# Optimization experiments

Hardware: AMD Instinct MI355X
Metric: run time of the kernel (lower is better)

The kernel has to match this reference:

```python
import jax, jax.numpy as jnp
import numpy as np


def setup_inputs() -> dict:
    key = jax.random.key(0)
    k1, k2, k3, k4 = jax.random.split(key, 4)
    TOKENS, IN_F, OUT_F = 4096, 4096, 11008
    x = jax.random.normal(k1, (TOKENS, IN_F), dtype=jnp.float32)
    # int8-valued weights stored in fp32 buffer, as in the torch module
    quantized_weight = jax.random.randint(k2, (OUT_F, IN_F), -128, 128).astype(jnp.float32)
    # per-output-channel scales, positive, small (like max|w|/127)
    weight_scales = (jax.random.uniform(k3, (OUT_F, 1), dtype=jnp.float32) * 0.03 + 0.001)
    bias = jax.random.normal(k4, (OUT_F,), dtype=jnp.float32)
    return {"x": x, "quantized_weight": quantized_weight,
            "weight_scales": weight_scales, "bias": bias}


def reference(x, quantized_weight, weight_scales, bias):
    # dequantize: per-channel scale broadcast over in_features
    weight = quantized_weight * weight_scales  # [out, in]
    # F.linear: x @ weight.T + bias
    return jnp.dot(x, weight.T) + bias
```

## Files before the change

kernel.cpp:

```cpp
#include <hip/hip_runtime.h>
#include <hip/hip_bf16.h>


typedef __attribute__((ext_vector_type(4))) int   i32x4;
typedef __attribute__((ext_vector_type(4))) float f32x4;
typedef __attribute__((ext_vector_type(4))) unsigned int u32x4;

__device__ static inline unsigned int pack4(int q0, int q1, int q2, int q3) {
    return (unsigned)(q0 & 255) | ((unsigned)(q1 & 255) << 8) |
           ((unsigned)(q2 & 255) << 16) | ((unsigned)(q3 & 255) << 24);
}

__global__ void w_to_i8(const float* __restrict__ in,
                        u32x4* __restrict__ out, long n16) {
    const long stride = (long)gridDim.x * blockDim.x;
    for (long i = (long)blockIdx.x * blockDim.x + threadIdx.x; i < n16; i += stride) {
        const f32x4* p = reinterpret_cast<const f32x4*>(in) + i * 4;
        u32x4 o;
#pragma unroll
        for (int v = 0; v < 4; ++v) {
            f32x4 f = p[v];
            o[v] = pack4(__float2int_rn(f[0]), __float2int_rn(f[1]),
                         __float2int_rn(f[2]), __float2int_rn(f[3]));
        }
        out[i] = o;
    }
}

__global__ void x_quant_i8(const float* __restrict__ x,
                           unsigned int* __restrict__ xq,
                           float* __restrict__ sx, int K) {
    const int row = blockIdx.x;
    const int tid = threadIdx.x;
    const float* xr = x + (size_t)row * K;
    float m = 0.f;
    for (int b = tid * 16; b < K; b += blockDim.x * 16) {
        const f32x4* p = (const f32x4*)(xr + b);
#pragma unroll
        for (int v = 0; v < 4; ++v) {
            f32x4 f = p[v];
            m = fmaxf(m, fmaxf(fmaxf(fabsf(f[0]), fabsf(f[1])),
                               fmaxf(fabsf(f[2]), fabsf(f[3]))));
        }
    }
#pragma unroll
    for (int off = 32; off; off >>= 1) m = fmaxf(m, __shfl_xor(m, off));
    __shared__ float red[8];
    if ((tid & 63) == 0) red[tid >> 6] = m;
    __syncthreads();
    const int nw = blockDim.x >> 6;
    m = red[0];
    for (int i = 1; i < nw; ++i) m = fmaxf(m, red[i]);
    const float inv = (m > 0.f) ? 127.0f / m : 0.f;
    if (tid == 0) sx[row] = m * (1.0f / 127.0f);
    for (int b = tid * 16; b < K; b += blockDim.x * 16) {
        const f32x4* p = (const f32x4*)(xr + b);
        u32x4 o;
#pragma unroll
        for (int v = 0; v < 4; ++v) {
            f32x4 f = p[v];
            int q0 = min(127, max(-127, __float2int_rn(f[0] * inv)));
            int q1 = min(127, max(-127, __float2int_rn(f[1] * inv)));
            int q2 = min(127, max(-127, __float2int_rn(f[2] * inv)));
            int q3 = min(127, max(-127, __float2int_rn(f[3] * inv)));
            o[v] = pack4(q0, q1, q2, q3);
        }
        *reinterpret_cast<u32x4*>((char*)xq + (size_t)row * K + b) = o;
    }
}


#define GLOAD16(src, dst) __builtin_amdgcn_global_load_lds( \
    (const __attribute__((address_space(1))) void*)(src),   \
    (__attribute__((address_space(3))) void*)(dst), 16, 0, 0)

#define FENCE() asm volatile("" ::: "memory")
#define BAR()  do { FENCE(); __builtin_amdgcn_s_barrier(); FENCE(); } while (0)
#define WAIT_VM(n) asm volatile("s_waitcnt vmcnt(" #n ")" ::: "memory")
#define WAIT_LGKM0() asm volatile("s_waitcnt lgkmcnt(0)" ::: "memory")
#define SCHED0() __builtin_amdgcn_sched_barrier(0)

__global__ __launch_bounds__(512, 2)
void qlinear_gemm_i8v2(const char* __restrict__ A,
                       const char* __restrict__ B,
                       const float* __restrict__ sx,
                       const float* __restrict__ scales,
                       const float* __restrict__ bias,
                       float* __restrict__ C,
                       int M, int N, int K, int nbx) {
    __shared__ __align__(128) char smem[131072];

    const int tid  = threadIdx.x;
    const int lane = tid & 63;
    const int wid  = tid >> 6;
    const int wr   = wid >> 2;
    const int wc   = wid & 3;

    const int nwg = gridDim.x;
    const int q = nwg >> 3, r = nwg & 7;
    const int xcd = blockIdx.x & 7, boff_ = blockIdx.x >> 3;
    const int swz = (xcd < r ? xcd * (q + 1) : r * (q + 1) + (xcd - r) * q) + boff_;
    const int bcol = swz % nbx;
    const int brow = swz / nbx;

    const char* Ag = A + (size_t)brow * 256 * K;
    const char* Bg = B + (size_t)bcol * 256 * K;

    size_t sA[2], sB[2];
#pragma unroll
    for (int g = 0; g < 2; ++g) {
        const int c = tid + g * 512, rl = c >> 3, j = c & 7;
        const int rowA = ((rl >> 6) << 7) + (rl & 63);
        const int rowB = ((rl >> 5) << 6) + (rl & 31);
        sA[g] = (size_t)rowA * K + ((j ^ (rl & 7)) << 4);
        sB[g] = (size_t)rowB * K + ((j ^ (rl & 7)) << 4);
    }
    const int ld0 = tid * 16;

    auto stageA = [&](int rg, int h, int t) {
        const char* G = Ag + (size_t)h * 64 * K + (size_t)t * 128;
        char* base = smem + rg * 32768 + h * 16384;
        GLOAD16(G + sA[0], base + ld0);
        GLOAD16(G + sA[1], base + ld0 + 8192);
    };
    auto stageB = [&](int rg, int h, int t) {
        const char* G = Bg + (size_t)h * 32 * K + (size_t)t * 128;
        char* base = smem + 65536 + rg * 32768 + h * 16384;
        GLOAD16(G + sB[0], base + ld0);
        GLOAD16(G + sB[1], base + ld0 + 8192);
    };

    const int px0 = (((lane >> 4) ^ (lane & 7)) << 4);
    const int px1 = (((4 + (lane >> 4)) ^ (lane & 7)) << 4);
    const int arow = (wr * 64 + (lane & 15)) * 128;
    const int brw  = (wc * 32 + (lane & 15)) * 128;

    i32x4 acc[8][4] = {};
    i32x4 a0[8], a1[8], b0[4], b1[4];

    auto rdA = [&](int rg, int mh, i32x4 (&d)[8]) {
        const char* p = smem + rg * 32768 + mh * 16384 + arow;
#pragma unroll
        for (int i = 0; i < 4; ++i) {
            d[i * 2]     = *(const i32x4*)(p + i * 2048 + px0);
            d[i * 2 + 1] = *(const i32x4*)(p + i * 2048 + px1);
        }
    };
    auto rdB = [&](int rg, int nh, i32x4 (&d)[4]) {
        const char* p = smem + 65536 + rg * 32768 + nh * 16384 + brw;
#pragma unroll
        for (int n = 0; n < 2; ++n) {
            d[n * 2]     = *(const i32x4*)(p + n * 2048 + px0);
            d[n * 2 + 1] = *(const i32x4*)(p + n * 2048 + px1);
        }
    };
    auto mfma16 = [&](const i32x4 (&a)[8], const i32x4 (&b)[4], int mh, int nh) {
#pragma unroll
        for (int i = 0; i < 4; ++i)
#pragma unroll
            for (int n = 0; n < 2; ++n) {
                i32x4& ac = acc[mh * 4 + i][nh * 2 + n];
                ac = __builtin_amdgcn_mfma_i32_16x16x64_i8(a[i * 2], b[n * 2], ac, 0, 0, 0);
                ac = __builtin_amdgcn_mfma_i32_16x16x64_i8(a[i * 2 + 1], b[n * 2 + 1], ac, 0, 0, 0);
            }
    };

    const int NT = K / 128;

    stageA(0, 0, 0); stageB(0, 0, 0); stageA(0, 1, 0); stageB(0, 1, 0);
    stageA(1, 0, 1); stageB(1, 0, 1);
    WAIT_VM(4); BAR();

    for (int t = 0; t < NT - 2; ++t) {
        const int c = t & 1, o = c ^ 1;
        stageA(o, 1, t + 1); stageB(o, 1, t + 1);
        rdA(c, 0, a0); rdB(c, 0, b0); rdB(c, 1, b1);
        WAIT_LGKM0(); SCHED0();
        __builtin_amdgcn_s_setprio(1);
        mfma16(a0, b0, 0, 0);
        mfma16(a0, b1, 0, 1);
        __builtin_amdgcn_s_setprio(0);
        BAR();
        stageA(c, 0, t + 2); stageB(c, 0, t + 2);
        rdA(c, 1, a1);
        WAIT_LGKM0(); SCHED0();
        __builtin_amdgcn_s_setprio(1);
        mfma16(a1, b0, 1, 0);
        mfma16(a1, b1, 1, 1);
        __builtin_amdgcn_s_setprio(0);
        WAIT_VM(4);
        BAR();
    }
    {
        const int c = (NT - 2) & 1, o = c ^ 1;
        stageA(o, 1, NT - 1); stageB(o, 1, NT - 1);
        rdA(c, 0, a0); rdB(c, 0, b0); rdB(c, 1, b1);
        WAIT_LGKM0(); SCHED0();
        __builtin_amdgcn_s_setprio(1);
        mfma16(a0, b0, 0, 0);
        mfma16(a0, b1, 0, 1);
        __builtin_amdgcn_s_setprio(0);
        BAR();
        rdA(c, 1, a1);
        WAIT_LGKM0(); SCHED0();
        __builtin_amdgcn_s_setprio(1);
        mfma16(a1, b0, 1, 0);
        mfma16(a1, b1, 1, 1);
        __builtin_amdgcn_s_setprio(0);
        WAIT_VM(0);
        BAR();
    }
    {
        const int c = (NT - 1) & 1;
        rdA(c, 0, a0); rdB(c, 0, b0); rdB(c, 1, b1);
        WAIT_LGKM0(); SCHED0();
        mfma16(a0, b0, 0, 0);
        mfma16(a0, b1, 0, 1);
        rdA(c, 1, a1);
        WAIT_LGKM0(); SCHED0();
        mfma16(a1, b0, 1, 0);
        mfma16(a1, b1, 1, 1);
    }

    const int lc  = lane & 15;
    const int lr4 = (lane >> 4) * 4;
    float sarr[4], barr[4];
#pragma unroll
    for (int ni = 0; ni < 4; ++ni) {
        const int n = bcol * 256 + wc * 64 + (ni >> 1) * 32 + (ni & 1) * 16 + lc;
        sarr[ni] = scales[n];
        barr[ni] = bias[n];
    }
#pragma unroll
    for (int mi = 0; mi < 8; ++mi) {
        const int mb = brow * 256 + wr * 128 + (mi >> 2) * 64 + (mi & 3) * 16 + lr4;
#pragma unroll
        for (int j = 0; j < 4; ++j) {
            const size_t rowoff = (size_t)(mb + j) * N;
            const float sm = sx[mb + j];
#pragma unroll
            for (int ni = 0; ni < 4; ++ni) {
                const int n = bcol * 256 + wc * 64 + (ni >> 1) * 32 + (ni & 1) * 16 + lc;
                C[rowoff + n] = fmaf((float)acc[mi][ni][j], sm * sarr[ni], barr[ni]);
            }
        }
    }
}

__global__ void qlinear_fallback(const float* __restrict__ A,
                                 const float* __restrict__ B,
                                 const float* __restrict__ scales,
                                 const float* __restrict__ bias,
                                 float* __restrict__ C, int M, int N, int K) {
    __shared__ float As[16][17], Bs[16][17];
    const int tx = threadIdx.x, ty = threadIdx.y;
    const int row = blockIdx.y * 16 + ty;
    const int col = blockIdx.x * 16 + tx;
    float acc = 0.f;
    for (int k0 = 0; k0 < K; k0 += 16) {
        As[ty][tx] = A[(long)row * K + k0 + tx];
        Bs[ty][tx] = B[(long)(blockIdx.x * 16 + ty) * K + k0 + tx];
        __syncthreads();
#pragma unroll
        for (int kk = 0; kk < 16; ++kk) acc += As[ty][kk] * Bs[tx][kk];
        __syncthreads();
    }
    C[(long)row * N + col] = fmaf(acc, scales[col], bias[col]);
}

extern "C" void kernel_launch(void* const* d_in, const int* in_sizes, int n_in,
                              void* d_out, int out_size, void* d_ws, size_t ws_size,
                              hipStream_t stream) {
    const float* x      = (const float*)d_in[0];
    const float* w      = (const float*)d_in[1];
    const float* scales = (const float*)d_in[2];
    const float* bias   = (const float*)d_in[3];
    float* out = (float*)d_out;

    const int N = in_sizes[2];
    const int K = (int)((long)in_sizes[1] / N);
    const int M = (int)((long)in_sizes[0] / K);

    const size_t need = (size_t)M * K + (size_t)N * K + (size_t)M * 4;
    const bool ok = (ws_size >= need) && (M % 256) == 0 && (N % 256) == 0 &&
                    (K % 128) == 0 && (K / 128) >= 3 && (K % 16) == 0;

    if (ok) {
        char* xq = (char*)d_ws;
        char* wq = xq + (size_t)M * K;
        float* sxbuf = (float*)(wq + (size_t)N * K);

        x_quant_i8<<<M, 256, 0, stream>>>(x, (unsigned int*)xq, sxbuf, K);
        w_to_i8<<<2048, 256, 0, stream>>>(w, (u32x4*)wq, (long)N * K / 16);

        const int nbx = N / 256;
        const int nwg = (M / 256) * nbx;
        qlinear_gemm_i8v2<<<nwg, 512, 0, stream>>>(xq, wq, sxbuf, scales, bias,
                                                   out, M, N, K, nbx);
    } else {
        dim3 grid(N / 16, M / 16), blk(16, 16);
        qlinear_fallback<<<grid, blk, 0, stream>>>(x, w, scales, bias, out, M, N, K);
    }
}
```

Baseline: 254.8 us.

## Switch int8 GEMM inner loop to 32x32x32 MFMA tiles

Replaces the 16x16x64 int8 MFMA instructions with 32x32x32 int8 MFMAs, restructuring the LDS read pattern, register fragments and accumulator layout (i32x16) to match. The epilogue is rewritten for the 32x32 output lane mapping and loads the row scales as a vector. The aim is fewer MFMA issues and LDS reads per unit of work and better operand reuse. It changes register pressure and the LDS access pattern, which could affect bank conflicts and occupancy at the 512x2 launch bounds.

Measured after the change: 284.0 us. +11.5%, slower.

```diff
diff --git a/kernel.cpp b/kernel.cpp
--- a/kernel.cpp
+++ b/kernel.cpp
@@ -2,9 +2,10 @@
 #include <hip/hip_bf16.h>
 
 
-typedef __attribute__((ext_vector_type(4))) int   i32x4;
-typedef __attribute__((ext_vector_type(4))) float f32x4;
-typedef __attribute__((ext_vector_type(4))) unsigned int u32x4;
+typedef __attribute__((ext_vector_type(4)))  int   i32x4;
+typedef __attribute__((ext_vector_type(16))) int   i32x16;
+typedef __attribute__((ext_vector_type(4)))  float f32x4;
+typedef __attribute__((ext_vector_type(4)))  unsigned int u32x4;
 
 __device__ static inline unsigned int pack4(int q0, int q1, int q2, int q3) {
     return (unsigned)(q0 & 255) | ((unsigned)(q1 & 255) << 8) |
@@ -81,13 +82,13 @@
 #define SCHED0() __builtin_amdgcn_sched_barrier(0)
 
 __global__ __launch_bounds__(512, 2)
-void qlinear_gemm_i8v2(const char* __restrict__ A,
-                       const char* __restrict__ B,
-                       const float* __restrict__ sx,
-                       const float* __restrict__ scales,
-                       const float* __restrict__ bias,
-                       float* __restrict__ C,
-                       int M, int N, int K, int nbx) {
+void qlinear_gemm_i8x32(const char* __restrict__ A,
+                        const char* __restrict__ B,
+                        const float* __restrict__ sx,
+                        const float* __restrict__ scales,
+                        const float* __restrict__ bias,
+                        float* __restrict__ C,
+                        int M, int N, int K, int nbx) {
     __shared__ __align__(128) char smem[131072];
 
     const int tid  = threadIdx.x;
@@ -130,39 +131,39 @@
         GLOAD16(G + sB[1], base + ld0 + 8192);
     };
 
-    const int px0 = (((lane >> 4) ^ (lane & 7)) << 4);
-    const int px1 = (((4 + (lane >> 4)) ^ (lane & 7)) << 4);
-    const int arow = (wr * 64 + (lane & 15)) * 128;
-    const int brw  = (wc * 32 + (lane & 15)) * 128;
-
-    i32x4 acc[8][4] = {};
-    i32x4 a0[8], a1[8], b0[4], b1[4];
-
-    auto rdA = [&](int rg, int mh, i32x4 (&d)[8]) {
-        const char* p = smem + rg * 32768 + mh * 16384 + arow;
-#pragma unroll
-        for (int i = 0; i < 4; ++i) {
-            d[i * 2]     = *(const i32x4*)(p + i * 2048 + px0);
-            d[i * 2 + 1] = *(const i32x4*)(p + i * 2048 + px1);
-        }
-    };
-    auto rdB = [&](int rg, int nh, i32x4 (&d)[4]) {
-        const char* p = smem + 65536 + rg * 32768 + nh * 16384 + brw;
-#pragma unroll
-        for (int n = 0; n < 2; ++n) {
-            d[n * 2]     = *(const i32x4*)(p + n * 2048 + px0);
-            d[n * 2 + 1] = *(const i32x4*)(p + n * 2048 + px1);
-        }
-    };
-    auto mfma16 = [&](const i32x4 (&a)[8], const i32x4 (&b)[4], int mh, int nh) {
-#pragma unroll
-        for (int i = 0; i < 4; ++i)
-#pragma unroll
-            for (int n = 0; n < 2; ++n) {
-                i32x4& ac = acc[mh * 4 + i][nh * 2 + n];
-                ac = __builtin_amdgcn_mfma_i32_16x16x64_i8(a[i * 2], b[n * 2], ac, 0, 0, 0);
-                ac = __builtin_amdgcn_mfma_i32_16x16x64_i8(a[i * 2 + 1], b[n * 2 + 1], ac, 0, 0, 0);
-            }
+    const int l31 = lane & 31;
+    const int lhi = lane >> 5;
+    const int l7  = lane & 7;
+    int pk[4];
+#pragma unroll
+    for (int ks = 0; ks < 4; ++ks) pk[ks] = ((ks * 2 + lhi) ^ l7) << 4;
+
+    i32x16 acc[4][2] = {};
+    i32x4 am0[4], am1[4], am2[4], am3[4];
+    i32x4 bn0[4], bn1[4];
+
+    auto rdA32 = [&](int rg, int mh, int j, i32x4 (&d)[4]) {
+        const char* p = smem + rg * 32768 + mh * 16384 +
+                        (wr * 64 + j * 32 + l31) * 128;
+#pragma unroll
+        for (int ks = 0; ks < 4; ++ks) d[ks] = *(const i32x4*)(p + pk[ks]);
+    };
+    auto rdB32 = [&](int rg, int n, i32x4 (&d)[4]) {
+        const char* p = smem + 65536 + rg * 32768 + n * 16384 +
+                        (wc * 32 + l31) * 128;
+#pragma unroll
+        for (int ks = 0; ks < 4; ++ks) d[ks] = *(const i32x4*)(p + pk[ks]);
+    };
+    auto mfmaPh = [&](const i32x4 (&x0)[4], const i32x4 (&x1)[4], int mbase) {
+        __builtin_amdgcn_s_setprio(1);
+#pragma unroll
+        for (int ks = 0; ks < 4; ++ks) {
+            acc[mbase][0]     = __builtin_amdgcn_mfma_i32_32x32x32_i8(x0[ks], bn0[ks], acc[mbase][0], 0, 0, 0);
+            acc[mbase][1]     = __builtin_amdgcn_mfma_i32_32x32x32_i8(x0[ks], bn1[ks], acc[mbase][1], 0, 0, 0);
+            acc[mbase + 1][0] = __builtin_amdgcn_mfma_i32_32x32x32_i8(x1[ks], bn0[ks], acc[mbase + 1][0], 0, 0, 0);
+            acc[mbase + 1][1] = __builtin_amdgcn_mfma_i32_32x32x32_i8(x1[ks], bn1[ks], acc[mbase + 1][1], 0, 0, 0);
+        }
+        __builtin_amdgcn_s_setprio(0);
     };
 
     const int NT = K / 128;
@@ -174,74 +175,61 @@
     for (int t = 0; t < NT - 2; ++t) {
         const int c = t & 1, o = c ^ 1;
         stageA(o, 1, t + 1); stageB(o, 1, t + 1);
-        rdA(c, 0, a0); rdB(c, 0, b0); rdB(c, 1, b1);
-        WAIT_LGKM0(); SCHED0();
-        __builtin_amdgcn_s_setprio(1);
-        mfma16(a0, b0, 0, 0);
-        mfma16(a0, b1, 0, 1);
-        __builtin_amdgcn_s_setprio(0);
+        rdA32(c, 0, 0, am0); rdA32(c, 0, 1, am1);
+        rdB32(c, 0, bn0);    rdB32(c, 1, bn1);
+        WAIT_LGKM0(); SCHED0();
+        mfmaPh(am0, am1, 0);
         BAR();
         stageA(c, 0, t + 2); stageB(c, 0, t + 2);
-        rdA(c, 1, a1);
-        WAIT_LGKM0(); SCHED0();
-        __builtin_amdgcn_s_setprio(1);
-        mfma16(a1, b0, 1, 0);
-        mfma16(a1, b1, 1, 1);
-        __builtin_amdgcn_s_setprio(0);
+        rdA32(c, 1, 0, am2); rdA32(c, 1, 1, am3);
+        WAIT_LGKM0(); SCHED0();
+        mfmaPh(am2, am3, 2);
         WAIT_VM(4);
         BAR();
     }
     {
         const int c = (NT - 2) & 1, o = c ^ 1;
         stageA(o, 1, NT - 1); stageB(o, 1, NT - 1);
-        rdA(c, 0, a0); rdB(c, 0, b0); rdB(c, 1, b1);
-        WAIT_LGKM0(); SCHED0();
-        __builtin_amdgcn_s_setprio(1);
-        mfma16(a0, b0, 0, 0);
-        mfma16(a0, b1, 0, 1);
-        __builtin_amdgcn_s_setprio(0);
-        BAR();
-        rdA(c, 1, a1);
-        WAIT_LGKM0(); SCHED0();
-        __builtin_amdgcn_s_setprio(1);
-        mfma16(a1, b0, 1, 0);
-        mfma16(a1, b1, 1, 1);
-        __builtin_amdgcn_s_setprio(0);
+        rdA32(c, 0, 0, am0); rdA32(c, 0, 1, am1);
+        rdB32(c, 0, bn0);    rdB32(c, 1, bn1);
+        WAIT_LGKM0(); SCHED0();
+        mfmaPh(am0, am1, 0);
+        BAR();
+        rdA32(c, 1, 0, am2); rdA32(c, 1, 1, am3);
+        WAIT_LGKM0(); SCHED0();
+        mfmaPh(am2, am3, 2);
         WAIT_VM(0);
         BAR();
     }
     {
         const int c = (NT - 1) & 1;
-        rdA(c, 0, a0); rdB(c, 0, b0); rdB(c, 1, b1);
-        WAIT_LGKM0(); SCHED0();
-        mfma16(a0, b0, 0, 0);
-        mfma16(a0, b1, 0, 1);
-        rdA(c, 1, a1);
-        WAIT_LGKM0(); SCHED0();
-        mfma16(a1, b0, 1, 0);
-        mfma16(a1, b1, 1, 1);
-    }
-
-    const int lc  = lane & 15;
-    const int lr4 = (lane >> 4) * 4;
-    float sarr[4], barr[4];
-#pragma unroll
-    for (int ni = 0; ni < 4; ++ni) {
-        const int n = bcol * 256 + wc * 64 + (ni >> 1) * 32 + (ni & 1) * 16 + lc;
-        sarr[ni] = scales[n];
-        barr[ni] = bias[n];
-    }
-#pragma unroll
-    for (int mi = 0; mi < 8; ++mi) {
-        const int mb = brow * 256 + wr * 128 + (mi >> 2) * 64 + (mi & 3) * 16 + lr4;
-#pragma unroll
-        for (int j = 0; j < 4; ++j) {
-            const size_t rowoff = (size_t)(mb + j) * N;
-            const float sm = sx[mb + j];
-#pragma unroll
-            for (int ni = 0; ni < 4; ++ni) {
-                const int n = bcol * 256 + wc * 64 + (ni >> 1) * 32 + (ni & 1) * 16 + lc;
-                C[rowoff + n] = fmaf((float)acc[mi][ni][j], sm * sarr[ni], barr[ni]);
+        rdA32(c, 0, 0, am0); rdA32(c, 0, 1, am1);
+        rdB32(c, 0, bn0);    rdB32(c, 1, bn1);
+        WAIT_LGKM0(); SCHED0();
+        mfmaPh(am0, am1, 0);
+        rdA32(c, 1, 0, am2); rdA32(c, 1, 1, am3);
+        WAIT_LGKM0(); SCHED0();
+        mfmaPh(am2, am3, 2);
+    }
+
+    const int rofs = (lane >> 5) * 4;
+#pragma unroll
+    for (int n = 0; n < 2; ++n) {
+        const int col = bcol * 256 + wc * 64 + n * 32 + l31;
+        const float s  = scales[col];
+        const float bz = bias[col];
+#pragma unroll
+        for (int m = 0; m < 4; ++m) {
+            const int rbase = brow * 256 + wr * 128 + m * 32 + rofs;
+#pragma unroll
+            for (int g = 0; g < 4; ++g) {
+                const int rowg = rbase + g * 8;
+                const f32x4 sxv = *(const f32x4*)&sx[rowg];
+#pragma unroll
+                for (int qq = 0; qq < 4; ++qq) {
+                    C[(size_t)(rowg + qq) * N + col] =
+                        fmaf((float)acc[m][n][g * 4 + qq], sxv[qq] * s, bz);
+                }
             }
         }
     }
@@ -295,8 +283,8 @@
 
         const int nbx = N / 256;
         const int nwg = (M / 256) * nbx;
-        qlinear_gemm_i8v2<<<nwg, 512, 0, stream>>>(xq, wq, sxbuf, scales, bias,
-                                                   out, M, N, K, nbx);
+        qlinear_gemm_i8x32<<<nwg, 512, 0, stream>>>(xq, wq, sxbuf, scales, bias,
+                                                    out, M, N, K, nbx);
     } else {
         dim3 grid(N / 16, M / 16), blk(16, 16);
         qlinear_fallback<<<grid, blk, 0, stream>>>(x, w, scales, bias, out, M, N, K);
```
